# Optimization experiments

Hardware: AMD Instinct MI355X
Metric: run time of the kernel (lower is better)

Reference implementation:

```python
import jax, jax.numpy as jnp
import numpy as np

GROUP_SIZE = 64
SHARED_EXPERT_WEIGHT = 1.0
# FP4 E2M1 codebook: sign bit + {0,.5,1,1.5,2,3,4,6}
FP4_TABLE = jnp.array([0.0, 0.5, 1.0, 1.5, 2.0, 3.0, 4.0, 6.0,
                       -0.0, -0.5, -1.0, -1.5, -2.0, -3.0, -4.0, -6.0], dtype=jnp.float32)


def dequant_fp4(packed, scales, group_size=GROUP_SIZE):
    """packed: [..., K//8, N] int32 (8 nibbles along K per word),
    scales: [..., K//group_size, N] -> dequantized [..., K, N] fp32."""
    shifts = (jnp.arange(8, dtype=jnp.int32) * 4)[:, None]          # [8,1]
    nib = jnp.right_shift(packed[..., :, None, :], shifts) & 0xF     # [..., K//8, 8, N]
    w = FP4_TABLE[nib]
    K = packed.shape[-2] * 8
    w = w.reshape(packed.shape[:-2] + (K, packed.shape[-1]))         # [..., K, N]
    s = jnp.repeat(scales, group_size, axis=-2)                      # [..., K, N]
    return w * s


def setup_inputs() -> dict:
    key = jax.random.key(0)
    ks = jax.random.split(key, 12)
    T, K, I, E, TOPK = 2048, 2048, 1024, 8, 2
    GS = GROUP_SIZE
    MAXI = 2**31 - 1
    u = lambda k, shp: jax.random.uniform(k, shp, jnp.float32, 0.005, 0.02)
    probs = jax.random.uniform(ks[10], (T, TOPK), jnp.float32)
    probs = probs / probs.sum(-1, keepdims=True)
    return {
        "hidden_states": jax.random.normal(ks[0], (T, K), jnp.float32),
        "gate_up_weight_packed": jax.random.randint(ks[1], (E, K // 8, 2 * I), 0, MAXI, jnp.int32),
        "gate_up_scales": u(ks[2], (E, K // GS, 2 * I)),
        "down_weight_packed": jax.random.randint(ks[3], (E, I // 8, K), 0, MAXI, jnp.int32),
        "down_scales": u(ks[4], (E, I // GS, K)),
        "shared_gate_up_packed": jax.random.randint(ks[5], (K // 8, 2 * I), 0, MAXI, jnp.int32),
        "shared_gate_up_scales": u(ks[6], (K // GS, 2 * I)),
        "shared_down_packed": jax.random.randint(ks[7], (I // 8, K), 0, MAXI, jnp.int32),
        "shared_down_scales": u(ks[8], (I // GS, K)),
        "expert_ids": jax.random.randint(ks[9], (T, TOPK), 0, E, jnp.int32),
        "expert_probs": probs,
    }


def reference(hidden_states, gate_up_weight_packed, gate_up_scales,
              down_weight_packed, down_scales,
              shared_gate_up_packed, shared_gate_up_scales,
              shared_down_packed, shared_down_scales,
              expert_ids, expert_probs):
    x = hidden_states                                                # [T, K]
    E = gate_up_weight_packed.shape[0]
    # --- routed experts: dequant + grouped GEMM over all tokens per expert ---
    Wgu = dequant_fp4(gate_up_weight_packed, gate_up_scales)         # [E, K, 2I]
    Wd = dequant_fp4(down_weight_packed, down_scales)                # [E, I, K]
    h = jnp.einsum('tk,ekn->etn', x, Wgu)                            # [E, T, 2I]
    gate, up = jnp.split(h, 2, axis=-1)
    act = jax.nn.silu(gate) * up                                     # [E, T, I]
    y = jnp.einsum('eti,eik->etk', act, Wd)                          # [E, T, K]
    # combine[t,e] = sum over top-k slots routed to e of prob
    one_hot = jax.nn.one_hot(expert_ids, E, dtype=x.dtype)           # [T, topk, E]
    combine = jnp.einsum('tk,tke->te', expert_probs, one_hot)        # [T, E]
    out = jnp.einsum('te,etk->tk', combine, y)                       # [T, K]
    # --- shared expert (always applied, weighted) ---
    Wgu_s = dequant_fp4(shared_gate_up_packed, shared_gate_up_scales)  # [K, 2I]
    Wd_s = dequant_fp4(shared_down_packed, shared_down_scales)         # [I, K]
    hs = x @ Wgu_s
    gs, us = jnp.split(hs, 2, axis=-1)
    shared_out = (jax.nn.silu(gs) * us) @ Wd_s
    return out + SHARED_EXPERT_WEIGHT * shared_out
```

## Files before the change

kernel.cpp:

```cpp
#include <hip/hip_runtime.h>
#include <hip/hip_bf16.h>

#define T_TOK 2048
#define K_DIM 2048
#define I_DIM 1024
#define NE    8
#define TOPK  2
#define GS    64

#define NSLOT  (T_TOK * TOPK)
#define TOTROW (NSLOT + T_TOK)
#define MAXITEM 55
#define DQD_Y   144

typedef __attribute__((ext_vector_type(8))) short short8;
typedef __attribute__((ext_vector_type(4))) float f32x4;

#define WS_XB   ((size_t)65536)
#define WS_ACT  (WS_XB  + (size_t)2048 * 2048 * 2)
#define WS_Y    (WS_ACT + (size_t)TOTROW * 1024 * 2)
#define WS_WGU  (WS_Y   + (size_t)TOTROW * 2048 * 2)
#define WS_WD   (WS_WGU + (size_t)9 * 2048 * 2048 * 2)


__device__ __forceinline__ unsigned pack2(float a, float b) {
    __hip_bfloat162 h = __float22bfloat162_rn(make_float2(a, b));
    return *reinterpret_cast<unsigned*>(&h);
}

__device__ __forceinline__ unsigned scale2(unsigned p, float s) {
    float f0 = __uint_as_float(p << 16) * s;
    float f1 = __uint_as_float(p & 0xFFFF0000u) * s;
    return pack2(f0, f1);
}

__device__ __forceinline__ float bf2f(ushort h) {
    return __uint_as_float((unsigned)h << 16);
}

__device__ __forceinline__ void dq_word(unsigned w, float s, unsigned o[4]) {
    unsigned lo  = w & 0x0F0F0F0Fu;
    unsigned hi  = (w >> 4) & 0x0F0F0F0Fu;
    unsigned mlo = lo & 0x07070707u, mhi = hi & 0x07070707u;
    unsigned Hlo = __builtin_amdgcn_perm(0x40404040u, 0x3F3F3F00u, mlo);
    unsigned Hhi = __builtin_amdgcn_perm(0x40404040u, 0x3F3F3F00u, mhi);
    unsigned Llo = __builtin_amdgcn_perm(0xC0804000u, 0xC0800000u, mlo);
    unsigned Lhi = __builtin_amdgcn_perm(0xC0804000u, 0xC0800000u, mhi);
    Hlo |= (lo & 0x08080808u) << 4;
    Hhi |= (hi & 0x08080808u) << 4;
    unsigned e01 = __builtin_amdgcn_perm(Hlo, Llo, 0x05010400u);
    unsigned e23 = __builtin_amdgcn_perm(Hlo, Llo, 0x07030602u);
    unsigned o01 = __builtin_amdgcn_perm(Hhi, Lhi, 0x05010400u);
    unsigned o23 = __builtin_amdgcn_perm(Hhi, Lhi, 0x07030602u);
    o[0] = scale2(e01, s); o[1] = scale2(e23, s);
    o[2] = scale2(o01, s); o[3] = scale2(o23, s);
}

__device__ __forceinline__ void dq4(const int* __restrict__ wp, const float* __restrict__ sc,
                                    ushort* __restrict__ op, int KW, int kb, int nb, int tid) {
    const int N = 2048;
    int n   = nb * 64 + (tid & 63);
    int kwt = kb * 16 + (tid >> 6) * 4;
    float s = sc[(size_t)(kwt >> 3) * N + n];
    ushort* dst = op + (size_t)n * (KW * 8) + kwt * 8;
    #pragma unroll
    for (int j = 0; j < 4; j++) {
        unsigned w = (unsigned)wp[(size_t)(kwt + j) * N + n];
        unsigned o[4]; dq_word(w, s, o);
        *(int4*)(dst + j * 8) = make_int4(o[0], o[1], o[2], o[3]);
    }
}

__device__ __forceinline__ void gld16(const void* g, void* l) {
    __builtin_amdgcn_global_load_lds(
        (const __attribute__((address_space(1))) unsigned*)g,
        (__attribute__((address_space(3))) unsigned*)l, 16, 0, 0);
}

#define GU_BLK  (9 * 512)
#define PREP_BLK 2048
#define FRONT_GRID (GU_BLK + PREP_BLK + 1)

__global__ __launch_bounds__(256) void k_front(
        const float* __restrict__ x, ushort* __restrict__ xb,
        const int* __restrict__ gup, const float* __restrict__ gus,
        const int* __restrict__ sup, const float* __restrict__ sus,
        ushort* __restrict__ wgu_t,
        const int* __restrict__ eids, const float* __restrict__ probs,
        int* __restrict__ gcnt, int* __restrict__ gbase,
        int* __restrict__ tileCnt, int* __restrict__ tileE, int* __restrict__ tileM,
        int* __restrict__ tok, int* __restrict__ inv) {
    int id = blockIdx.x;
    int tid = threadIdx.x;

    if (id < GU_BLK) {
        int e = id >> 9, rem = id & 511;
        int kb = rem & 15, nb = rem >> 4;
        const int* wp; const float* sc;
        if (e < NE) { wp = gup + (size_t)e * 256 * 2048; sc = gus + (size_t)e * 32 * 2048; }
        else        { wp = sup; sc = sus; }
        dq4(wp, sc, wgu_t + (size_t)e * 2048 * 2048, 256, kb, nb, tid);
    } else if (id < GU_BLK + PREP_BLK) {
        int idx = (id - GU_BLK) * 256 + tid;
        const float4* p = (const float4*)(x + (size_t)idx * 8);
        float4 f0 = p[0], f1 = p[1];
        unsigned u0 = pack2(f0.x, f0.z);
        unsigned u1 = pack2(f1.x, f1.z);
        unsigned u2 = pack2(f0.y, f0.w);
        unsigned u3 = pack2(f1.y, f1.w);
        *(int4*)(xb + (size_t)idx * 8) = make_int4(u0, u1, u2, u3);
    } else {
        __shared__ int lcnt[NE], lbase[NE], lcur[NE];
        if (tid < NE) lcnt[tid] = 0;
        __syncthreads();
        for (int i = tid; i < NSLOT; i += 256)
            atomicAdd(&lcnt[eids[i]], 1);
        __syncthreads();
        if (tid == 0) {
            int acc = 0;
            for (int e = 0; e < NE; e++) { lbase[e] = acc; acc += lcnt[e]; }
        }
        __syncthreads();
        if (tid < NE) lcur[tid] = lbase[tid];
        __syncthreads();
        for (int i = tid; i < NSLOT; i += 256) {
            int e = eids[i];
            int pos = atomicAdd(&lcur[e], 1);
            tok[pos] = i >> 1;
            inv[i] = pos;
        }
        for (int t = tid; t < T_TOK; t += 256)
            tok[NSLOT + t] = t;
        if (tid < NE) { gcnt[tid] = lcnt[tid]; gbase[tid] = lbase[tid]; }
        if (tid == 0) {
            gcnt[NE] = T_TOK; gbase[NE] = NSLOT;
            int nt = 0;
            for (int e = 0; e < NE + 1; e++) {
                int c = (e < NE) ? lcnt[e] : T_TOK;
                for (int m = 0; m < c; m += 128) { tileE[nt] = e; tileM[nt] = m; nt++; }
            }
            *tileCnt = nt;
            for (int i = nt; i < 64; i++) { tileE[i] = 0; tileM[i] = 0; }
        }
    }
}

__global__ __launch_bounds__(256) void k_gemm_gateup(
        const ushort* __restrict__ xb, const ushort* __restrict__ wgu_t,
        const int* __restrict__ dwp, const float* __restrict__ dsc,
        const int* __restrict__ sdp, const float* __restrict__ sds,
        ushort* __restrict__ wd_t,
        const int* __restrict__ gcnt, const int* __restrict__ gbase,
        const int* __restrict__ tileCnt, const int* __restrict__ tileE,
        const int* __restrict__ tileM,
        const int* __restrict__ tokid, ushort* __restrict__ act) {
    int tid = threadIdx.x;
    if (blockIdx.y >= MAXITEM) {
        int id2 = (blockIdx.y - MAXITEM) * 16 + blockIdx.x;
        int e = id2 >> 8, rem = id2 & 255;
        int kb = rem & 7, nb = rem >> 3;
        const int* wp; const float* sc;
        if (e < NE) { wp = dwp + (size_t)e * 128 * 2048; sc = dsc + (size_t)e * 16 * 2048; }
        else        { wp = sdp; sc = sds; }
        dq4(wp, sc, wd_t + (size_t)e * 2048 * 1024, 128, kb, nb, tid);
        return;
    }
    int item = blockIdx.y;
    if (item >= *tileCnt) return;
    int e = tileE[item], m0 = tileM[item];
    int cnt = gcnt[e], base = gbase[e];
    int n0 = blockIdx.x * 64;
    const ushort* wt = wgu_t + (size_t)e * 2048 * K_DIM;

    __shared__ __align__(16) ushort xs[128 * 64];
    __shared__ __align__(16) ushort bs[128 * 64];
    __shared__ int ltok[128];

    int lane = tid & 63, wv = tid >> 6;
    int lid = lane & 15, quad = lane >> 4;
    int wr = wv >> 1, wc = wv & 1;
    int l8 = lane >> 3, l7 = lane & 7;
    int chunk = (l7 ^ l8) * 8;

    if (tid < 128) ltok[tid] = (m0 + tid < cnt) ? tokid[base + m0 + tid] : 0;
    __syncthreads();

    const ushort* aSrc[4]; const ushort* bSrc[4];
    #pragma unroll
    for (int it = 0; it < 4; it++) {
        int rA = wv * 32 + it * 8 + l8;
        aSrc[it] = xb + (size_t)ltok[rA] * K_DIM + chunk;
        int h = rA >> 6, j = rA & 63;
        int col = (j < 32) ? (n0 + h * 32 + j) : (I_DIM + n0 + h * 32 + (j - 32));
        bSrc[it] = wt + (size_t)col * K_DIM + chunk;
    }

    f32x4 acc[4][4] = {};

    for (int k0 = 0; k0 < K_DIM; k0 += 64) {
        #pragma unroll
        for (int it = 0; it < 4; it++) {
            gld16(aSrc[it] + k0, &xs[(wv * 4 + it) * 512]);
            gld16(bSrc[it] + k0, &bs[(wv * 4 + it) * 512]);
        }
        __syncthreads();
        #pragma unroll
        for (int ks = 0; ks < 2; ks++) {
            int slot = ((ks * 4 + quad) ^ l7) * 8;
            short8 a[4], b[4];
            #pragma unroll
            for (int mt = 0; mt < 4; mt++)
                a[mt] = *(const short8*)&xs[(wr * 64 + mt * 16 + lid) * 64 + slot];
            #pragma unroll
            for (int nt = 0; nt < 4; nt++)
                b[nt] = *(const short8*)&bs[(wc * 64 + nt * 16 + lid) * 64 + slot];
            #pragma unroll
            for (int mt = 0; mt < 4; mt++)
                #pragma unroll
                for (int nt = 0; nt < 4; nt++)
                    acc[mt][nt] = __builtin_amdgcn_mfma_f32_16x16x32_bf16(
                        a[mt], b[nt], acc[mt][nt], 0, 0, 0);
        }
        __syncthreads();
    }

    int c7 = lid & 7;
    int delta = ((c7 >> 1) + ((c7 & 1) << 2)) - c7;
    #pragma unroll
    for (int mt = 0; mt < 4; mt++) {
        #pragma unroll
        for (int i = 0; i < 4; i++) {
            int row = wr * 64 + mt * 16 + quad * 4 + i;
            if (m0 + row < cnt) {
                size_t p = (size_t)(base + m0 + row);
                #pragma unroll
                for (int nt = 0; nt < 2; nt++) {
                    float g = acc[mt][nt][i], u = acc[mt][nt + 2][i];
                    float vv = g / (1.f + __expf(-g)) * u;
                    int ncol = n0 + wc * 32 + nt * 16 + lid;
                    __hip_bfloat16 hb = __float2bfloat16(vv);
                    act[p * I_DIM + ncol + delta] = *reinterpret_cast<ushort*>(&hb);
                }
            }
        }
    }
}

__global__ __launch_bounds__(256) void k_gemm_down(
        const ushort* __restrict__ actb, const ushort* __restrict__ wd_t,
        const int* __restrict__ gcnt, const int* __restrict__ gbase,
        const int* __restrict__ tileCnt, const int* __restrict__ tileE,
        const int* __restrict__ tileM,
        ushort* __restrict__ y) {
    int item = blockIdx.y;
    if (item >= *tileCnt) return;
    int e = tileE[item], m0 = tileM[item];
    int cnt = gcnt[e], base = gbase[e];
    int n0 = blockIdx.x * 128;
    const ushort* wt = wd_t + (size_t)e * 2048 * I_DIM;

    __shared__ __align__(16) ushort xs[128 * 64];
    __shared__ __align__(16) ushort bs[128 * 64];

    int tid = threadIdx.x;
    int lane = tid & 63, wv = tid >> 6;
    int lid = lane & 15, quad = lane >> 4;
    int wr = wv >> 1, wc = wv & 1;
    int l8 = lane >> 3, l7 = lane & 7;
    int chunk = (l7 ^ l8) * 8;

    const ushort* aSrc[4]; const ushort* bSrc[4];
    #pragma unroll
    for (int it = 0; it < 4; it++) {
        int rA = wv * 32 + it * 8 + l8;
        int rr = m0 + rA; if (rr >= cnt) rr = cnt - 1;
        aSrc[it] = actb + (size_t)(base + rr) * I_DIM + chunk;
        bSrc[it] = wt + (size_t)(n0 + rA) * I_DIM + chunk;
    }

    f32x4 acc[4][4] = {};

    for (int i0 = 0; i0 < I_DIM; i0 += 64) {
        #pragma unroll
        for (int it = 0; it < 4; it++) {
            gld16(aSrc[it] + i0, &xs[(wv * 4 + it) * 512]);
            gld16(bSrc[it] + i0, &bs[(wv * 4 + it) * 512]);
        }
        __syncthreads();
        #pragma unroll
        for (int ks = 0; ks < 2; ks++) {
            int slot = ((ks * 4 + quad) ^ l7) * 8;
            short8 a[4], b[4];
            #pragma unroll
            for (int mt = 0; mt < 4; mt++)
                a[mt] = *(const short8*)&xs[(wr * 64 + mt * 16 + lid) * 64 + slot];
            #pragma unroll
            for (int nt = 0; nt < 4; nt++)
                b[nt] = *(const short8*)&bs[(wc * 64 + nt * 16 + lid) * 64 + slot];
            #pragma unroll
            for (int mt = 0; mt < 4; mt++)
                #pragma unroll
                for (int nt = 0; nt < 4; nt++)
                    acc[mt][nt] = __builtin_amdgcn_mfma_f32_16x16x32_bf16(
                        a[mt], b[nt], acc[mt][nt], 0, 0, 0);
        }
        __syncthreads();
    }

    #pragma unroll
    for (int mt = 0; mt < 4; mt++) {
        #pragma unroll
        for (int i = 0; i < 4; i++) {
            int row = wr * 64 + mt * 16 + quad * 4 + i;
            if (m0 + row < cnt) {
                ushort* yrow = y + (size_t)(base + m0 + row) * 2048 + n0 + wc * 64 + lid;
                #pragma unroll
                for (int nt = 0; nt < 4; nt++) {
                    __hip_bfloat16 hb = __float2bfloat16(acc[mt][nt][i]);
                    yrow[nt * 16] = *reinterpret_cast<ushort*>(&hb);
                }
            }
        }
    }
}

__global__ __launch_bounds__(256) void k_combine(
        const ushort* __restrict__ y, const int* __restrict__ inv,
        const float* __restrict__ prb, float* __restrict__ out) {
    int idx = blockIdx.x * 256 + threadIdx.x;
    int t = idx >> 8;
    int c = (idx & 255) * 8;
    int p0 = inv[2 * t], p1 = inv[2 * t + 1];
    float w0 = prb[2 * t], w1 = prb[2 * t + 1];
    int4 a = *(const int4*)(y + (size_t)p0 * 2048 + c);
    int4 b = *(const int4*)(y + (size_t)p1 * 2048 + c);
    int4 s = *(const int4*)(y + (size_t)(NSLOT + t) * 2048 + c);
    const ushort* au = (const ushort*)&a;
    const ushort* bu = (const ushort*)&b;
    const ushort* su = (const ushort*)&s;
    float o[8];
    #pragma unroll
    for (int j = 0; j < 8; j++)
        o[j] = w0 * bf2f(au[j]) + w1 * bf2f(bu[j]) + bf2f(su[j]);
    *(float4*)(out + (size_t)t * 2048 + c)     = *(float4*)&o[0];
    *(float4*)(out + (size_t)t * 2048 + c + 4) = *(float4*)&o[4];
}

extern "C" void kernel_launch(void* const* d_in, const int* in_sizes, int n_in,
                              void* d_out, int out_size, void* d_ws, size_t ws_size,
                              hipStream_t stream) {
    const float* x    = (const float*)d_in[0];
    const int*   gup  = (const int*)d_in[1];
    const float* gus  = (const float*)d_in[2];
    const int*   dwp  = (const int*)d_in[3];
    const float* dsc  = (const float*)d_in[4];
    const int*   sup  = (const int*)d_in[5];
    const float* sus  = (const float*)d_in[6];
    const int*   sdp  = (const int*)d_in[7];
    const float* sds  = (const float*)d_in[8];
    const int*   eids = (const int*)d_in[9];
    const float* prb  = (const float*)d_in[10];
    float* out = (float*)d_out;

    char*   ws      = (char*)d_ws;
    int*    gcnt    = (int*)(ws + 0);
    int*    gbase   = (int*)(ws + 64);
    int*    tileCnt = (int*)(ws + 128);
    int*    tileE   = (int*)(ws + 192);
    int*    tileM   = (int*)(ws + 448);
    int*    tok     = (int*)(ws + 1024);
    int*    inv     = (int*)(ws + 25600);
    ushort* xb      = (ushort*)(ws + WS_XB);
    ushort* act     = (ushort*)(ws + WS_ACT);
    ushort* y       = (ushort*)(ws + WS_Y);
    ushort* wgu_t   = (ushort*)(ws + WS_WGU);
    ushort* wd_t    = (ushort*)(ws + WS_WD);

    k_front<<<FRONT_GRID, 256, 0, stream>>>(
        x, xb, gup, gus, sup, sus, wgu_t,
        eids, prb, gcnt, gbase, tileCnt, tileE, tileM, tok, inv);
    k_gemm_gateup<<<dim3(I_DIM / 64, MAXITEM + DQD_Y), 256, 0, stream>>>(
        xb, wgu_t, dwp, dsc, sdp, sds, wd_t,
        gcnt, gbase, tileCnt, tileE, tileM, tok, act);
    k_gemm_down<<<dim3(K_DIM / 128, MAXITEM), 256, 0, stream>>>(
        act, wd_t, gcnt, gbase, tileCnt, tileE, tileM, y);
    k_combine<<<(T_TOK * K_DIM / 8) / 256, 256, 0, stream>>>(y, inv, prb, out);
}
```

Baseline: 254.7 us.

## Load MFMA operands directly from global memory, dropping LDS staging in both GEMMs

Both grouped GEMM kernels no longer stage A and B tiles through shared memory with global_load_lds and barriers. Each lane now loads its short8 MFMA fragments straight from global memory into registers. This removes the barriers and LDS traffic, but data that was shared across waves in a block is now fetched redundantly from global/L2 by each wave. Loads also lose their coalescing, since each lane reads 16 bytes from a different row.

```diff
diff --git a/kernel.cpp b/kernel.cpp
--- a/kernel.cpp
+++ b/kernel.cpp
@@ -69,12 +69,6 @@
         unsigned o[4]; dq_word(w, s, o);
         *(int4*)(dst + j * 8) = make_int4(o[0], o[1], o[2], o[3]);
     }
-}
-
-__device__ __forceinline__ void gld16(const void* g, void* l) {
-    __builtin_amdgcn_global_load_lds(
-        (const __attribute__((address_space(1))) unsigned*)g,
-        (__attribute__((address_space(3))) unsigned*)l, 16, 0, 0);
 }
 
 #define GU_BLK  (9 * 512)
@@ -172,56 +166,39 @@
     int n0 = blockIdx.x * 64;
     const ushort* wt = wgu_t + (size_t)e * 2048 * K_DIM;
 
-    __shared__ __align__(16) ushort xs[128 * 64];
-    __shared__ __align__(16) ushort bs[128 * 64];
-    __shared__ int ltok[128];
-
     int lane = tid & 63, wv = tid >> 6;
     int lid = lane & 15, quad = lane >> 4;
     int wr = wv >> 1, wc = wv & 1;
-    int l8 = lane >> 3, l7 = lane & 7;
-    int chunk = (l7 ^ l8) * 8;
-
-    if (tid < 128) ltok[tid] = (m0 + tid < cnt) ? tokid[base + m0 + tid] : 0;
-    __syncthreads();
-
-    const ushort* aSrc[4]; const ushort* bSrc[4];
-    #pragma unroll
-    for (int it = 0; it < 4; it++) {
-        int rA = wv * 32 + it * 8 + l8;
-        aSrc[it] = xb + (size_t)ltok[rA] * K_DIM + chunk;
-        int h = rA >> 6, j = rA & 63;
+
+    const ushort* aP[4]; const ushort* bP[4];
+    #pragma unroll
+    for (int mt = 0; mt < 4; mt++) {
+        int row = wr * 64 + mt * 16 + lid;
+        int t = (m0 + row < cnt) ? tokid[base + m0 + row] : 0;
+        aP[mt] = xb + (size_t)t * K_DIM + quad * 8;
+    }
+    #pragma unroll
+    for (int nt = 0; nt < 4; nt++) {
+        int br = wc * 64 + nt * 16 + lid;
+        int h = br >> 6, j = br & 63;
         int col = (j < 32) ? (n0 + h * 32 + j) : (I_DIM + n0 + h * 32 + (j - 32));
-        bSrc[it] = wt + (size_t)col * K_DIM + chunk;
+        bP[nt] = wt + (size_t)col * K_DIM + quad * 8;
     }
 
     f32x4 acc[4][4] = {};
-
-    for (int k0 = 0; k0 < K_DIM; k0 += 64) {
-        #pragma unroll
-        for (int it = 0; it < 4; it++) {
-            gld16(aSrc[it] + k0, &xs[(wv * 4 + it) * 512]);
-            gld16(bSrc[it] + k0, &bs[(wv * 4 + it) * 512]);
-        }
-        __syncthreads();
-        #pragma unroll
-        for (int ks = 0; ks < 2; ks++) {
-            int slot = ((ks * 4 + quad) ^ l7) * 8;
-            short8 a[4], b[4];
-            #pragma unroll
-            for (int mt = 0; mt < 4; mt++)
-                a[mt] = *(const short8*)&xs[(wr * 64 + mt * 16 + lid) * 64 + slot];
+    #pragma unroll 2
+    for (int k = 0; k < K_DIM; k += 32) {
+        short8 a[4], b[4];
+        #pragma unroll
+        for (int mt = 0; mt < 4; mt++) a[mt] = *(const short8*)(aP[mt] + k);
+        #pragma unroll
+        for (int nt = 0; nt < 4; nt++) b[nt] = *(const short8*)(bP[nt] + k);
+        #pragma unroll
+        for (int mt = 0; mt < 4; mt++)
             #pragma unroll
             for (int nt = 0; nt < 4; nt++)
-                b[nt] = *(const short8*)&bs[(wc * 64 + nt * 16 + lid) * 64 + slot];
-            #pragma unroll
-            for (int mt = 0; mt < 4; mt++)
-                #pragma unroll
-                for (int nt = 0; nt < 4; nt++)
-                    acc[mt][nt] = __builtin_amdgcn_mfma_f32_16x16x32_bf16(
-                        a[mt], b[nt], acc[mt][nt], 0, 0, 0);
-        }
-        __syncthreads();
+                acc[mt][nt] = __builtin_amdgcn_mfma_f32_16x16x32_bf16(
+                    a[mt], b[nt], acc[mt][nt], 0, 0, 0);
     }
 
     int c7 = lid & 7;
@@ -259,52 +236,38 @@
     int n0 = blockIdx.x * 128;
     const ushort* wt = wd_t + (size_t)e * 2048 * I_DIM;
 
-    __shared__ __align__(16) ushort xs[128 * 64];
-    __shared__ __align__(16) ushort bs[128 * 64];
-
     int tid = threadIdx.x;
     int lane = tid & 63, wv = tid >> 6;
     int lid = lane & 15, quad = lane >> 4;
     int wr = wv >> 1, wc = wv & 1;
-    int l8 = lane >> 3, l7 = lane & 7;
-    int chunk = (l7 ^ l8) * 8;
-
-    const ushort* aSrc[4]; const ushort* bSrc[4];
-    #pragma unroll
-    for (int it = 0; it < 4; it++) {
-        int rA = wv * 32 + it * 8 + l8;
-        int rr = m0 + rA; if (rr >= cnt) rr = cnt - 1;
-        aSrc[it] = actb + (size_t)(base + rr) * I_DIM + chunk;
-        bSrc[it] = wt + (size_t)(n0 + rA) * I_DIM + chunk;
+
+    const ushort* aP[4]; const ushort* bP[4];
+    #pragma unroll
+    for (int mt = 0; mt < 4; mt++) {
+        int row = m0 + wr * 64 + mt * 16 + lid;
+        if (row >= cnt) row = cnt - 1;
+        aP[mt] = actb + (size_t)(base + row) * I_DIM + quad * 8;
+    }
+    #pragma unroll
+    for (int nt = 0; nt < 4; nt++) {
+        int col = n0 + wc * 64 + nt * 16 + lid;
+        bP[nt] = wt + (size_t)col * I_DIM + quad * 8;
     }
 
     f32x4 acc[4][4] = {};
-
-    for (int i0 = 0; i0 < I_DIM; i0 += 64) {
-        #pragma unroll
-        for (int it = 0; it < 4; it++) {
-            gld16(aSrc[it] + i0, &xs[(wv * 4 + it) * 512]);
-            gld16(bSrc[it] + i0, &bs[(wv * 4 + it) * 512]);
-        }
-        __syncthreads();
-        #pragma unroll
-        for (int ks = 0; ks < 2; ks++) {
-            int slot = ((ks * 4 + quad) ^ l7) * 8;
-            short8 a[4], b[4];
-            #pragma unroll
-            for (int mt = 0; mt < 4; mt++)
-                a[mt] = *(const short8*)&xs[(wr * 64 + mt * 16 + lid) * 64 + slot];
+    #pragma unroll 2
+    for (int k = 0; k < I_DIM; k += 32) {
+        short8 a[4], b[4];
+        #pragma unroll
+        for (int mt = 0; mt < 4; mt++) a[mt] = *(const short8*)(aP[mt] + k);
+        #pragma unroll
+        for (int nt = 0; nt < 4; nt++) b[nt] = *(const short8*)(bP[nt] + k);
+        #pragma unroll
+        for (int mt = 0; mt < 4; mt++)
             #pragma unroll
             for (int nt = 0; nt < 4; nt++)
-                b[nt] = *(const short8*)&bs[(wc * 64 + nt * 16 + lid) * 64 + slot];
-            #pragma unroll
-            for (int mt = 0; mt < 4; mt++)
-                #pragma unroll
-                for (int nt = 0; nt < 4; nt++)
-                    acc[mt][nt] = __builtin_amdgcn_mfma_f32_16x16x32_bf16(
-                        a[mt], b[nt], acc[mt][nt], 0, 0, 0);
-        }
-        __syncthreads();
+                acc[mt][nt] = __builtin_amdgcn_mfma_f32_16x16x32_bf16(
+                    a[mt], b[nt], acc[mt][nt], 0, 0, 0);
     }
 
     #pragma unroll
```

Measured after the change: 516.6 us. 103% more time.

## Fuse four MoE kernels into one persistent cooperative kernel with grid syncs

Applied to the files above, without the earlier changes.

Merges the front (dequant, cast, routing), gate-up GEMM plus down-weight dequant, down GEMM, and combine kernels into a single persistent cooperative kernel. Blocks loop over work items, and stages are separated by grid.sync. This removes three kernel launches and the tail gaps between them. In exchange, the grid is capped at 256×occupancy blocks, register pressure from launch_bounds(256,3) may cause spills, and grid-wide barriers can idle blocks when stage work is unevenly spread.

```diff
diff --git a/kernel.cpp b/kernel.cpp
--- a/kernel.cpp
+++ b/kernel.cpp
@@ -1,5 +1,7 @@
 #include <hip/hip_runtime.h>
 #include <hip/hip_bf16.h>
+#include <hip/hip_cooperative_groups.h>
+namespace cg = cooperative_groups;
 
 #define T_TOK 2048
 #define K_DIM 2048
@@ -11,7 +13,6 @@
 #define NSLOT  (T_TOK * TOPK)
 #define TOTROW (NSLOT + T_TOK)
 #define MAXITEM 55
-#define DQD_Y   144
 
 typedef __attribute__((ext_vector_type(8))) short short8;
 typedef __attribute__((ext_vector_type(4))) float f32x4;
@@ -21,6 +22,15 @@
 #define WS_Y    (WS_ACT + (size_t)TOTROW * 1024 * 2)
 #define WS_WGU  (WS_Y   + (size_t)TOTROW * 2048 * 2)
 #define WS_WD   (WS_WGU + (size_t)9 * 2048 * 2048 * 2)
+
+#define GU_ITEMS   4608
+#define PREP_ITEMS 2048
+#define S0_ITEMS   (GU_ITEMS + PREP_ITEMS + 1)
+#define GEMM1_ITEMS (16 * MAXITEM)
+#define DQD_ITEMS   2304
+#define S1_ITEMS   (GEMM1_ITEMS + DQD_ITEMS)
+#define S2_ITEMS   (16 * MAXITEM)
+#define S3_ITEMS   2048
 
 
 __device__ __forceinline__ unsigned pack2(float a, float b) {
@@ -77,273 +87,262 @@
         (__attribute__((address_space(3))) unsigned*)l, 16, 0, 0);
 }
 
-#define GU_BLK  (9 * 512)
-#define PREP_BLK 2048
-#define FRONT_GRID (GU_BLK + PREP_BLK + 1)
-
-__global__ __launch_bounds__(256) void k_front(
-        const float* __restrict__ x, ushort* __restrict__ xb,
+__global__ __launch_bounds__(256, 3) void k_moe(
+        const float* __restrict__ x,
         const int* __restrict__ gup, const float* __restrict__ gus,
         const int* __restrict__ sup, const float* __restrict__ sus,
-        ushort* __restrict__ wgu_t,
-        const int* __restrict__ eids, const float* __restrict__ probs,
-        int* __restrict__ gcnt, int* __restrict__ gbase,
-        int* __restrict__ tileCnt, int* __restrict__ tileE, int* __restrict__ tileM,
-        int* __restrict__ tok, int* __restrict__ inv) {
-    int id = blockIdx.x;
-    int tid = threadIdx.x;
-
-    if (id < GU_BLK) {
-        int e = id >> 9, rem = id & 511;
-        int kb = rem & 15, nb = rem >> 4;
-        const int* wp; const float* sc;
-        if (e < NE) { wp = gup + (size_t)e * 256 * 2048; sc = gus + (size_t)e * 32 * 2048; }
-        else        { wp = sup; sc = sus; }
-        dq4(wp, sc, wgu_t + (size_t)e * 2048 * 2048, 256, kb, nb, tid);
-    } else if (id < GU_BLK + PREP_BLK) {
-        int idx = (id - GU_BLK) * 256 + tid;
-        const float4* p = (const float4*)(x + (size_t)idx * 8);
-        float4 f0 = p[0], f1 = p[1];
-        unsigned u0 = pack2(f0.x, f0.z);
-        unsigned u1 = pack2(f1.x, f1.z);
-        unsigned u2 = pack2(f0.y, f0.w);
-        unsigned u3 = pack2(f1.y, f1.w);
-        *(int4*)(xb + (size_t)idx * 8) = make_int4(u0, u1, u2, u3);
-    } else {
-        __shared__ int lcnt[NE], lbase[NE], lcur[NE];
-        if (tid < NE) lcnt[tid] = 0;
-        __syncthreads();
-        for (int i = tid; i < NSLOT; i += 256)
-            atomicAdd(&lcnt[eids[i]], 1);
-        __syncthreads();
-        if (tid == 0) {
-            int acc = 0;
-            for (int e = 0; e < NE; e++) { lbase[e] = acc; acc += lcnt[e]; }
-        }
-        __syncthreads();
-        if (tid < NE) lcur[tid] = lbase[tid];
-        __syncthreads();
-        for (int i = tid; i < NSLOT; i += 256) {
-            int e = eids[i];
-            int pos = atomicAdd(&lcur[e], 1);
-            tok[pos] = i >> 1;
-            inv[i] = pos;
-        }
-        for (int t = tid; t < T_TOK; t += 256)
-            tok[NSLOT + t] = t;
-        if (tid < NE) { gcnt[tid] = lcnt[tid]; gbase[tid] = lbase[tid]; }
-        if (tid == 0) {
-            gcnt[NE] = T_TOK; gbase[NE] = NSLOT;
-            int nt = 0;
-            for (int e = 0; e < NE + 1; e++) {
-                int c = (e < NE) ? lcnt[e] : T_TOK;
-                for (int m = 0; m < c; m += 128) { tileE[nt] = e; tileM[nt] = m; nt++; }
-            }
-            *tileCnt = nt;
-            for (int i = nt; i < 64; i++) { tileE[i] = 0; tileM[i] = 0; }
-        }
-    }
-}
-
-__global__ __launch_bounds__(256) void k_gemm_gateup(
-        const ushort* __restrict__ xb, const ushort* __restrict__ wgu_t,
         const int* __restrict__ dwp, const float* __restrict__ dsc,
         const int* __restrict__ sdp, const float* __restrict__ sds,
-        ushort* __restrict__ wd_t,
-        const int* __restrict__ gcnt, const int* __restrict__ gbase,
-        const int* __restrict__ tileCnt, const int* __restrict__ tileE,
-        const int* __restrict__ tileM,
-        const int* __restrict__ tokid, ushort* __restrict__ act) {
-    int tid = threadIdx.x;
-    if (blockIdx.y >= MAXITEM) {
-        int id2 = (blockIdx.y - MAXITEM) * 16 + blockIdx.x;
-        int e = id2 >> 8, rem = id2 & 255;
-        int kb = rem & 7, nb = rem >> 3;
-        const int* wp; const float* sc;
-        if (e < NE) { wp = dwp + (size_t)e * 128 * 2048; sc = dsc + (size_t)e * 16 * 2048; }
-        else        { wp = sdp; sc = sds; }
-        dq4(wp, sc, wd_t + (size_t)e * 2048 * 1024, 128, kb, nb, tid);
-        return;
-    }
-    int item = blockIdx.y;
-    if (item >= *tileCnt) return;
-    int e = tileE[item], m0 = tileM[item];
-    int cnt = gcnt[e], base = gbase[e];
-    int n0 = blockIdx.x * 64;
-    const ushort* wt = wgu_t + (size_t)e * 2048 * K_DIM;
+        const int* __restrict__ eids, const float* __restrict__ prb,
+        float* __restrict__ out, char* __restrict__ wsb) {
+    int*    gcnt    = (int*)(wsb + 0);
+    int*    gbase   = (int*)(wsb + 64);
+    int*    tileCnt = (int*)(wsb + 128);
+    int*    tileE   = (int*)(wsb + 192);
+    int*    tileM   = (int*)(wsb + 448);
+    int*    tok     = (int*)(wsb + 1024);
+    int*    inv     = (int*)(wsb + 25600);
+    ushort* xb      = (ushort*)(wsb + WS_XB);
+    ushort* act     = (ushort*)(wsb + WS_ACT);
+    ushort* y       = (ushort*)(wsb + WS_Y);
+    ushort* wgu_t   = (ushort*)(wsb + WS_WGU);
+    ushort* wd_t    = (ushort*)(wsb + WS_WD);
 
     __shared__ __align__(16) ushort xs[128 * 64];
     __shared__ __align__(16) ushort bs[128 * 64];
     __shared__ int ltok[128];
-
+    __shared__ int lcnt[NE], lbase[NE], lcur[NE];
+
+    cg::grid_group grid = cg::this_grid();
+    int tid = threadIdx.x;
+    int nb  = gridDim.x;
     int lane = tid & 63, wv = tid >> 6;
     int lid = lane & 15, quad = lane >> 4;
     int wr = wv >> 1, wc = wv & 1;
     int l8 = lane >> 3, l7 = lane & 7;
     int chunk = (l7 ^ l8) * 8;
 
-    if (tid < 128) ltok[tid] = (m0 + tid < cnt) ? tokid[base + m0 + tid] : 0;
-    __syncthreads();
-
-    const ushort* aSrc[4]; const ushort* bSrc[4];
-    #pragma unroll
-    for (int it = 0; it < 4; it++) {
-        int rA = wv * 32 + it * 8 + l8;
-        aSrc[it] = xb + (size_t)ltok[rA] * K_DIM + chunk;
-        int h = rA >> 6, j = rA & 63;
-        int col = (j < 32) ? (n0 + h * 32 + j) : (I_DIM + n0 + h * 32 + (j - 32));
-        bSrc[it] = wt + (size_t)col * K_DIM + chunk;
-    }
-
-    f32x4 acc[4][4] = {};
-
-    for (int k0 = 0; k0 < K_DIM; k0 += 64) {
+    for (int it = blockIdx.x; it < S0_ITEMS; it += nb) {
+        if (it < GU_ITEMS) {
+            int e = it >> 9, rem = it & 511;
+            int kb = rem & 15, nbl = rem >> 4;
+            const int* wp; const float* sc;
+            if (e < NE) { wp = gup + (size_t)e * 256 * 2048; sc = gus + (size_t)e * 32 * 2048; }
+            else        { wp = sup; sc = sus; }
+            dq4(wp, sc, wgu_t + (size_t)e * 2048 * 2048, 256, kb, nbl, tid);
+        } else if (it < GU_ITEMS + PREP_ITEMS) {
+            int idx = (it - GU_ITEMS) * 256 + tid;
+            const float4* p = (const float4*)(x + (size_t)idx * 8);
+            float4 f0 = p[0], f1 = p[1];
+            unsigned u0 = pack2(f0.x, f0.z);
+            unsigned u1 = pack2(f1.x, f1.z);
+            unsigned u2 = pack2(f0.y, f0.w);
+            unsigned u3 = pack2(f1.y, f1.w);
+            *(int4*)(xb + (size_t)idx * 8) = make_int4(u0, u1, u2, u3);
+        } else {
+            if (tid < NE) lcnt[tid] = 0;
+            __syncthreads();
+            for (int i = tid; i < NSLOT; i += 256)
+                atomicAdd(&lcnt[eids[i]], 1);
+            __syncthreads();
+            if (tid == 0) {
+                int acc = 0;
+                for (int e = 0; e < NE; e++) { lbase[e] = acc; acc += lcnt[e]; }
+            }
+            __syncthreads();
+            if (tid < NE) lcur[tid] = lbase[tid];
+            __syncthreads();
+            for (int i = tid; i < NSLOT; i += 256) {
+                int e = eids[i];
+                int pos = atomicAdd(&lcur[e], 1);
+                tok[pos] = i >> 1;
+                inv[i] = pos;
+            }
+            for (int t = tid; t < T_TOK; t += 256)
+                tok[NSLOT + t] = t;
+            if (tid < NE) { gcnt[tid] = lcnt[tid]; gbase[tid] = lbase[tid]; }
+            if (tid == 0) {
+                gcnt[NE] = T_TOK; gbase[NE] = NSLOT;
+                int nt = 0;
+                for (int e = 0; e < NE + 1; e++) {
+                    int c = (e < NE) ? lcnt[e] : T_TOK;
+                    for (int m = 0; m < c; m += 128) { tileE[nt] = e; tileM[nt] = m; nt++; }
+                }
+                *tileCnt = nt;
+                for (int i = nt; i < 64; i++) { tileE[i] = 0; tileM[i] = 0; }
+            }
+        }
+    }
+    __threadfence();
+    grid.sync();
+
+    int nTiles = *tileCnt;
+    for (int it = blockIdx.x; it < S1_ITEMS; it += nb) {
+        if (it < GEMM1_ITEMS) {
+            int item = it >> 4;
+            if (item >= nTiles) continue;
+            int e = tileE[item], m0 = tileM[item];
+            int cnt = gcnt[e], base = gbase[e];
+            int n0 = (it & 15) * 64;
+            const ushort* wt = wgu_t + (size_t)e * 2048 * K_DIM;
+
+            if (tid < 128) ltok[tid] = (m0 + tid < cnt) ? tok[base + m0 + tid] : 0;
+            __syncthreads();
+
+            const ushort* aSrc[4]; const ushort* bSrc[4];
+            #pragma unroll
+            for (int s4 = 0; s4 < 4; s4++) {
+                int rA = wv * 32 + s4 * 8 + l8;
+                aSrc[s4] = xb + (size_t)ltok[rA] * K_DIM + chunk;
+                int h = rA >> 6, j = rA & 63;
+                int col = (j < 32) ? (n0 + h * 32 + j) : (I_DIM + n0 + h * 32 + (j - 32));
+                bSrc[s4] = wt + (size_t)col * K_DIM + chunk;
+            }
+
+            f32x4 acc[4][4] = {};
+            for (int k0 = 0; k0 < K_DIM; k0 += 64) {
+                #pragma unroll
+                for (int s4 = 0; s4 < 4; s4++) {
+                    gld16(aSrc[s4] + k0, &xs[(wv * 4 + s4) * 512]);
+                    gld16(bSrc[s4] + k0, &bs[(wv * 4 + s4) * 512]);
+                }
+                __syncthreads();
+                #pragma unroll
+                for (int ks = 0; ks < 2; ks++) {
+                    int slot = ((ks * 4 + quad) ^ l7) * 8;
+                    short8 a[4], b[4];
+                    #pragma unroll
+                    for (int mt = 0; mt < 4; mt++)
+                        a[mt] = *(const short8*)&xs[(wr * 64 + mt * 16 + lid) * 64 + slot];
+                    #pragma unroll
+                    for (int nt = 0; nt < 4; nt++)
+                        b[nt] = *(const short8*)&bs[(wc * 64 + nt * 16 + lid) * 64 + slot];
+                    #pragma unroll
+                    for (int mt = 0; mt < 4; mt++)
+                        #pragma unroll
+                        for (int nt = 0; nt < 4; nt++)
+                            acc[mt][nt] = __builtin_amdgcn_mfma_f32_16x16x32_bf16(
+                                a[mt], b[nt], acc[mt][nt], 0, 0, 0);
+                }
+                __syncthreads();
+            }
+
+            int c7 = lid & 7;
+            int delta = ((c7 >> 1) + ((c7 & 1) << 2)) - c7;
+            #pragma unroll
+            for (int mt = 0; mt < 4; mt++) {
+                #pragma unroll
+                for (int i = 0; i < 4; i++) {
+                    int row = wr * 64 + mt * 16 + quad * 4 + i;
+                    if (m0 + row < cnt) {
+                        size_t p = (size_t)(base + m0 + row);
+                        #pragma unroll
+                        for (int nt = 0; nt < 2; nt++) {
+                            float g = acc[mt][nt][i], u = acc[mt][nt + 2][i];
+                            float vv = g / (1.f + __expf(-g)) * u;
+                            int ncol = n0 + wc * 32 + nt * 16 + lid;
+                            __hip_bfloat16 hb = __float2bfloat16(vv);
+                            act[p * I_DIM + ncol + delta] = *reinterpret_cast<ushort*>(&hb);
+                        }
+                    }
+                }
+            }
+        } else {
+            int id2 = it - GEMM1_ITEMS;
+            int e = id2 >> 8, rem = id2 & 255;
+            int kb = rem & 7, nbl = rem >> 3;
+            const int* wp; const float* sc;
+            if (e < NE) { wp = dwp + (size_t)e * 128 * 2048; sc = dsc + (size_t)e * 16 * 2048; }
+            else        { wp = sdp; sc = sds; }
+            dq4(wp, sc, wd_t + (size_t)e * 2048 * 1024, 128, kb, nbl, tid);
+        }
+    }
+    __threadfence();
+    grid.sync();
+
+    for (int it = blockIdx.x; it < S2_ITEMS; it += nb) {
+        int item = it >> 4;
+        if (item >= nTiles) continue;
+        int e = tileE[item], m0 = tileM[item];
+        int cnt = gcnt[e], base = gbase[e];
+        int n0 = (it & 15) * 128;
+        const ushort* wt = wd_t + (size_t)e * 2048 * I_DIM;
+
+        const ushort* aSrc[4]; const ushort* bSrc[4];
         #pragma unroll
-        for (int it = 0; it < 4; it++) {
-            gld16(aSrc[it] + k0, &xs[(wv * 4 + it) * 512]);
-            gld16(bSrc[it] + k0, &bs[(wv * 4 + it) * 512]);
-        }
-        __syncthreads();
+        for (int s4 = 0; s4 < 4; s4++) {
+            int rA = wv * 32 + s4 * 8 + l8;
+            int rr = m0 + rA; if (rr >= cnt) rr = cnt - 1;
+            aSrc[s4] = act + (size_t)(base + rr) * I_DIM + chunk;
+            bSrc[s4] = wt + (size_t)(n0 + rA) * I_DIM + chunk;
+        }
+
+        f32x4 acc[4][4] = {};
+        for (int i0 = 0; i0 < I_DIM; i0 += 64) {
+            #pragma unroll
+            for (int s4 = 0; s4 < 4; s4++) {
+                gld16(aSrc[s4] + i0, &xs[(wv * 4 + s4) * 512]);
+                gld16(bSrc[s4] + i0, &bs[(wv * 4 + s4) * 512]);
+            }
+            __syncthreads();
+            #pragma unroll
+            for (int ks = 0; ks < 2; ks++) {
+                int slot = ((ks * 4 + quad) ^ l7) * 8;
+                short8 a[4], b[4];
+                #pragma unroll
+                for (int mt = 0; mt < 4; mt++)
+                    a[mt] = *(const short8*)&xs[(wr * 64 + mt * 16 + lid) * 64 + slot];
+                #pragma unroll
+                for (int nt = 0; nt < 4; nt++)
+                    b[nt] = *(const short8*)&bs[(wc * 64 + nt * 16 + lid) * 64 + slot];
+                #pragma unroll
+                for (int mt = 0; mt < 4; mt++)
+                    #pragma unroll
+                    for (int nt = 0; nt < 4; nt++)
+                        acc[mt][nt] = __builtin_amdgcn_mfma_f32_16x16x32_bf16(
+                            a[mt], b[nt], acc[mt][nt], 0, 0, 0);
+            }
+            __syncthreads();
+        }
+
         #pragma unroll
-        for (int ks = 0; ks < 2; ks++) {
-            int slot = ((ks * 4 + quad) ^ l7) * 8;
-            short8 a[4], b[4];
-            #pragma unroll
-            for (int mt = 0; mt < 4; mt++)
-                a[mt] = *(const short8*)&xs[(wr * 64 + mt * 16 + lid) * 64 + slot];
-            #pragma unroll
-            for (int nt = 0; nt < 4; nt++)
-                b[nt] = *(const short8*)&bs[(wc * 64 + nt * 16 + lid) * 64 + slot];
-            #pragma unroll
-            for (int mt = 0; mt < 4; mt++)
-                #pragma unroll
-                for (int nt = 0; nt < 4; nt++)
-                    acc[mt][nt] = __builtin_amdgcn_mfma_f32_16x16x32_bf16(
-                        a[mt], b[nt], acc[mt][nt], 0, 0, 0);
-        }
-        __syncthreads();
-    }
-
-    int c7 = lid & 7;
-    int delta = ((c7 >> 1) + ((c7 & 1) << 2)) - c7;
-    #pragma unroll
-    for (int mt = 0; mt < 4; mt++) {
+        for (int mt = 0; mt < 4; mt++) {
+            #pragma unroll
+            for (int i = 0; i < 4; i++) {
+                int row = wr * 64 + mt * 16 + quad * 4 + i;
+                if (m0 + row < cnt) {
+                    ushort* yrow = y + (size_t)(base + m0 + row) * 2048 + n0 + wc * 64 + lid;
+                    #pragma unroll
+                    for (int nt = 0; nt < 4; nt++) {
+                        __hip_bfloat16 hb = __float2bfloat16(acc[mt][nt][i]);
+                        yrow[nt * 16] = *reinterpret_cast<ushort*>(&hb);
+                    }
+                }
+            }
+        }
+    }
+    __threadfence();
+    grid.sync();
+
+    for (int it = blockIdx.x; it < S3_ITEMS; it += nb) {
+        int idx = it * 256 + tid;
+        int t = idx >> 8;
+        int c = (idx & 255) * 8;
+        int p0 = inv[2 * t], p1 = inv[2 * t + 1];
+        float w0 = prb[2 * t], w1 = prb[2 * t + 1];
+        int4 a = *(const int4*)(y + (size_t)p0 * 2048 + c);
+        int4 b = *(const int4*)(y + (size_t)p1 * 2048 + c);
+        int4 s = *(const int4*)(y + (size_t)(NSLOT + t) * 2048 + c);
+        const ushort* au = (const ushort*)&a;
+        const ushort* bu = (const ushort*)&b;
+        const ushort* su = (const ushort*)&s;
+        float o[8];
         #pragma unroll
-        for (int i = 0; i < 4; i++) {
-            int row = wr * 64 + mt * 16 + quad * 4 + i;
-            if (m0 + row < cnt) {
-                size_t p = (size_t)(base + m0 + row);
-                #pragma unroll
-                for (int nt = 0; nt < 2; nt++) {
-                    float g = acc[mt][nt][i], u = acc[mt][nt + 2][i];
-                    float vv = g / (1.f + __expf(-g)) * u;
-                    int ncol = n0 + wc * 32 + nt * 16 + lid;
-                    __hip_bfloat16 hb = __float2bfloat16(vv);
-                    act[p * I_DIM + ncol + delta] = *reinterpret_cast<ushort*>(&hb);
-                }
-            }
-        }
-    }
-}
-
-__global__ __launch_bounds__(256) void k_gemm_down(
-        const ushort* __restrict__ actb, const ushort* __restrict__ wd_t,
-        const int* __restrict__ gcnt, const int* __restrict__ gbase,
-        const int* __restrict__ tileCnt, const int* __restrict__ tileE,
-        const int* __restrict__ tileM,
-        ushort* __restrict__ y) {
-    int item = blockIdx.y;
-    if (item >= *tileCnt) return;
-    int e = tileE[item], m0 = tileM[item];
-    int cnt = gcnt[e], base = gbase[e];
-    int n0 = blockIdx.x * 128;
-    const ushort* wt = wd_t + (size_t)e * 2048 * I_DIM;
-
-    __shared__ __align__(16) ushort xs[128 * 64];
-    __shared__ __align__(16) ushort bs[128 * 64];
-
-    int tid = threadIdx.x;
-    int lane = tid & 63, wv = tid >> 6;
-    int lid = lane & 15, quad = lane >> 4;
-    int wr = wv >> 1, wc = wv & 1;
-    int l8 = lane >> 3, l7 = lane & 7;
-    int chunk = (l7 ^ l8) * 8;
-
-    const ushort* aSrc[4]; const ushort* bSrc[4];
-    #pragma unroll
-    for (int it = 0; it < 4; it++) {
-        int rA = wv * 32 + it * 8 + l8;
-        int rr = m0 + rA; if (rr >= cnt) rr = cnt - 1;
-        aSrc[it] = actb + (size_t)(base + rr) * I_DIM + chunk;
-        bSrc[it] = wt + (size_t)(n0 + rA) * I_DIM + chunk;
-    }
-
-    f32x4 acc[4][4] = {};
-
-    for (int i0 = 0; i0 < I_DIM; i0 += 64) {
-        #pragma unroll
-        for (int it = 0; it < 4; it++) {
-            gld16(aSrc[it] + i0, &xs[(wv * 4 + it) * 512]);
-            gld16(bSrc[it] + i0, &bs[(wv * 4 + it) * 512]);
-        }
-        __syncthreads();
-        #pragma unroll
-        for (int ks = 0; ks < 2; ks++) {
-            int slot = ((ks * 4 + quad) ^ l7) * 8;
-            short8 a[4], b[4];
-            #pragma unroll
-            for (int mt = 0; mt < 4; mt++)
-                a[mt] = *(const short8*)&xs[(wr * 64 + mt * 16 + lid) * 64 + slot];
-            #pragma unroll
-            for (int nt = 0; nt < 4; nt++)
-                b[nt] = *(const short8*)&bs[(wc * 64 + nt * 16 + lid) * 64 + slot];
-            #pragma unroll
-            for (int mt = 0; mt < 4; mt++)
-                #pragma unroll
-                for (int nt = 0; nt < 4; nt++)
-                    acc[mt][nt] = __builtin_amdgcn_mfma_f32_16x16x32_bf16(
-                        a[mt], b[nt], acc[mt][nt], 0, 0, 0);
-        }
-        __syncthreads();
-    }
-
-    #pragma unroll
-    for (int mt = 0; mt < 4; mt++) {
-        #pragma unroll
-        for (int i = 0; i < 4; i++) {
-            int row = wr * 64 + mt * 16 + quad * 4 + i;
-            if (m0 + row < cnt) {
-                ushort* yrow = y + (size_t)(base + m0 + row) * 2048 + n0 + wc * 64 + lid;
-                #pragma unroll
-                for (int nt = 0; nt < 4; nt++) {
-                    __hip_bfloat16 hb = __float2bfloat16(acc[mt][nt][i]);
-                    yrow[nt * 16] = *reinterpret_cast<ushort*>(&hb);
-                }
-            }
-        }
-    }
-}
-
-__global__ __launch_bounds__(256) void k_combine(
-        const ushort* __restrict__ y, const int* __restrict__ inv,
-        const float* __restrict__ prb, float* __restrict__ out) {
-    int idx = blockIdx.x * 256 + threadIdx.x;
-    int t = idx >> 8;
-    int c = (idx & 255) * 8;
-    int p0 = inv[2 * t], p1 = inv[2 * t + 1];
-    float w0 = prb[2 * t], w1 = prb[2 * t + 1];
-    int4 a = *(const int4*)(y + (size_t)p0 * 2048 + c);
-    int4 b = *(const int4*)(y + (size_t)p1 * 2048 + c);
-    int4 s = *(const int4*)(y + (size_t)(NSLOT + t) * 2048 + c);
-    const ushort* au = (const ushort*)&a;
-    const ushort* bu = (const ushort*)&b;
-    const ushort* su = (const ushort*)&s;
-    float o[8];
-    #pragma unroll
-    for (int j = 0; j < 8; j++)
-        o[j] = w0 * bf2f(au[j]) + w1 * bf2f(bu[j]) + bf2f(su[j]);
-    *(float4*)(out + (size_t)t * 2048 + c)     = *(float4*)&o[0];
-    *(float4*)(out + (size_t)t * 2048 + c + 4) = *(float4*)&o[4];
+        for (int j = 0; j < 8; j++)
+            o[j] = w0 * bf2f(au[j]) + w1 * bf2f(bu[j]) + bf2f(su[j]);
+        *(float4*)(out + (size_t)t * 2048 + c)     = *(float4*)&o[0];
+        *(float4*)(out + (size_t)t * 2048 + c + 4) = *(float4*)&o[4];
+    }
 }
 
 extern "C" void kernel_launch(void* const* d_in, const int* in_sizes, int n_in,
@@ -361,28 +360,17 @@
     const int*   eids = (const int*)d_in[9];
     const float* prb  = (const float*)d_in[10];
     float* out = (float*)d_out;
-
-    char*   ws      = (char*)d_ws;
-    int*    gcnt    = (int*)(ws + 0);
-    int*    gbase   = (int*)(ws + 64);
-    int*    tileCnt = (int*)(ws + 128);
-    int*    tileE   = (int*)(ws + 192);
-    int*    tileM   = (int*)(ws + 448);
-    int*    tok     = (int*)(ws + 1024);
-    int*    inv     = (int*)(ws + 25600);
-    ushort* xb      = (ushort*)(ws + WS_XB);
-    ushort* act     = (ushort*)(ws + WS_ACT);
-    ushort* y       = (ushort*)(ws + WS_Y);
-    ushort* wgu_t   = (ushort*)(ws + WS_WGU);
-    ushort* wd_t    = (ushort*)(ws + WS_WD);
-
-    k_front<<<FRONT_GRID, 256, 0, stream>>>(
-        x, xb, gup, gus, sup, sus, wgu_t,
-        eids, prb, gcnt, gbase, tileCnt, tileE, tileM, tok, inv);
-    k_gemm_gateup<<<dim3(I_DIM / 64, MAXITEM + DQD_Y), 256, 0, stream>>>(
-        xb, wgu_t, dwp, dsc, sdp, sds, wd_t,
-        gcnt, gbase, tileCnt, tileE, tileM, tok, act);
-    k_gemm_down<<<dim3(K_DIM / 128, MAXITEM), 256, 0, stream>>>(
-        act, wd_t, gcnt, gbase, tileCnt, tileE, tileM, y);
-    k_combine<<<(T_TOK * K_DIM / 8) / 256, 256, 0, stream>>>(y, inv, prb, out);
-}
+    char*  wsb = (char*)d_ws;
+
+    int maxb = 0;
+    hipOccupancyMaxActiveBlocksPerMultiprocessor(&maxb, k_moe, 256, 0);
+    if (maxb < 1) maxb = 1;
+    if (maxb > 4) maxb = 4;
+    int grid = 256 * maxb;
+
+    void* args[] = { (void*)&x, (void*)&gup, (void*)&gus, (void*)&sup, (void*)&sus,
+                     (void*)&dwp, (void*)&dsc, (void*)&sdp, (void*)&sds,
+                     (void*)&eids, (void*)&prb, (void*)&out, (void*)&wsb };
+    hipLaunchCooperativeKernel((const void*)k_moe, dim3(grid), dim3(256),
+                               args, 0, stream);
+}
```

After: 568.1 us. +123.1%, slower.
